# Performance work log

Measured on AMD Instinct MI355X. Metric: run time of the kernel, lower is better.

Reference implementation:

```python
import jax, jax.numpy as jnp
import numpy as np

C_S, C_Z, C_H, H, PQ, PV = 384, 128, 16, 12, 4, 8
B, N = 1, 512
W_C = (2.0 / (9.0 * PQ)) ** 0.5
W_L = (1.0 / 3.0) ** 0.5
OUT_IN = H * C_Z + H * C_H + H * PV * 3 + H * PV  # 2112


def setup_inputs() -> dict:
    key = jax.random.key(0)
    ks = jax.random.split(key, 16)
    s_i = jax.random.normal(ks[0], (B, N, C_S), jnp.float32)
    z_ij = jax.random.normal(ks[1], (B, N, N, C_Z), jnp.float32)
    # random rotation matrices via QR
    raw = jax.random.normal(ks[2], (B, N, 3, 3), jnp.float32)
    q, r = jnp.linalg.qr(raw)
    rots = q * jnp.sign(jnp.diagonal(r, axis1=-2, axis2=-1))[..., None, :]
    trans = jax.random.normal(ks[3], (B, N, 3), jnp.float32)
    sc = lambda fan_in: 1.0 / np.sqrt(fan_in)
    Wq = jax.random.normal(ks[4], (C_S, H * C_H), jnp.float32) * sc(C_S)
    Wk = jax.random.normal(ks[5], (C_S, H * C_H), jnp.float32) * sc(C_S)
    Wv = jax.random.normal(ks[6], (C_S, H * C_H), jnp.float32) * sc(C_S)
    Wqp = jax.random.normal(ks[7], (C_S, H * PQ * 3), jnp.float32) * sc(C_S)
    Wkp = jax.random.normal(ks[8], (C_S, H * PQ * 3), jnp.float32) * sc(C_S)
    Wvp = jax.random.normal(ks[9], (C_S, H * PV * 3), jnp.float32) * sc(C_S)
    Wb = jax.random.normal(ks[10], (C_Z, H), jnp.float32) * sc(C_Z)
    gamma = jax.random.normal(ks[11], (1, 1, 1, H), jnp.float32)
    Wout = jax.random.normal(ks[12], (OUT_IN, C_S), jnp.float32) * sc(OUT_IN)
    bout = jnp.zeros((C_S,), jnp.float32)
    return dict(s_i=s_i, z_ij=z_ij, rots=rots, trans=trans, Wq=Wq, Wk=Wk, Wv=Wv,
                Wqp=Wqp, Wkp=Wkp, Wvp=Wvp, Wb=Wb, gamma=gamma, Wout=Wout, bout=bout)


def reference(s_i, z_ij, rots, trans, Wq, Wk, Wv, Wqp, Wkp, Wvp, Wb, gamma, Wout, bout):
    b, n = s_i.shape[0], s_i.shape[1]
    q_h = (s_i @ Wq).reshape(b, n, H, C_H)
    k_h = (s_i @ Wk).reshape(b, n, H, C_H)
    v_h = (s_i @ Wv).reshape(b, n, H, C_H)
    q_hp = (s_i @ Wqp).reshape(b, n, H, PQ, 3)
    k_hp = (s_i @ Wkp).reshape(b, n, H, PQ, 3)
    v_hp = (s_i @ Wvp).reshape(b, n, H, PV, 3)
    b_ij = z_ij @ Wb  # (b,i,j,h)

    t = trans[:, :, None, None, :]  # (b,i,1,1,3)
    apply = lambda x: jnp.einsum('bixy,bihpy->bihpx', rots, x) + t
    inv_apply = lambda x: jnp.einsum('bixy,bihpx->bihpy', rots, x - t)

    qg = apply(q_hp)  # (b,i,h,p,3) global frame
    kg = apply(k_hp)
    # pairwise rigid point distance term: (b,i,j,h)
    diff = qg[:, :, None] - kg[:, None]  # (b,i,j,h,p,3)
    dist2 = jnp.sum(diff * diff, axis=(-1, -2))

    a_s = jnp.einsum('bihd,bjhd->bijh', q_h, k_h) / (C_H ** 0.5)
    a_rigid = (W_C / 2.0) * gamma * dist2
    a = jax.nn.softmax(W_L * (a_s + b_ij - a_rigid), axis=-2)  # softmax over j

    o_hat = jnp.einsum('bijh,bijd->bihd', a, z_ij)
    o = jnp.einsum('bijh,bjhd->bihd', a, v_h)
    vg = apply(v_hp)  # (b,j,h,p,3)
    o_hp = inv_apply(jnp.einsum('bijh,bjhpx->bihpx', a, vg))  # (b,i,h,pv,3)
    o_hp_norm = jnp.sqrt(jnp.sum(o_hp * o_hp, axis=-1))  # (b,i,h,pv)

    cat = jnp.concatenate([
        o_hat.reshape(b, n, H * C_Z),
        o.reshape(b, n, H * C_H),
        o_hp.reshape(b, n, H * PV * 3),
        o_hp_norm.reshape(b, n, H * PV),
    ], axis=-1)
    return cat @ Wout + bout
```

## Files before the change

### kernel.cpp

```cpp
#include <hip/hip_runtime.h>
#include <hip/hip_bf16.h>
#include <math.h>

#define NRES 512
#define CS   384
#define CZ   128
#define NH   12
#define PW   1152
#define JB   64
#define NCH  8
#define PSTRIDE32 1040
#define KS   6
#define KAW  352

static constexpr float WL_F      = 0.57735026918962576f;
static constexpr float HALF_WC_F = 0.11785113019775792f;

typedef __attribute__((ext_vector_type(8))) short short8v;
typedef __attribute__((ext_vector_type(4))) float floatx4;

__device__ __forceinline__ ushort f2b(float f) {
    union { float f; uint u; } v; v.f = f;
    return (ushort)((v.u + 0x7FFFu + ((v.u >> 16) & 1u)) >> 16);
}
__device__ __forceinline__ float b2f(ushort b) {
    union { uint u; float f; } v; v.u = ((uint)b) << 16; return v.f;
}

__global__ __launch_bounds__(256) void k_prep(
    const float* __restrict__ Wb, const float* __restrict__ Wout,
    ushort* __restrict__ wbt16, ushort* __restrict__ woT)
{
    __shared__ ushort tile[64][72];
    const int bx = blockIdx.x;
    if (bx < 198) {
        const int k0 = (bx % 33) * 64, c0 = (bx / 33) * 64;
        for (int idx = threadIdx.x; idx < 4096; idx += 256) {
            const int r = idx >> 6, c = idx & 63;
            tile[r][c] = f2b(Wout[(size_t)(k0 + r) * 384 + c0 + c]);
        }
        __syncthreads();
        for (int idx = threadIdx.x; idx < 4096; idx += 256) {
            const int c = idx >> 6, r = idx & 63;
            woT[(size_t)(c0 + c) * 2112 + k0 + r] = tile[r][c];
        }
    } else {
        for (int idx = threadIdx.x; idx < 16 * 128; idx += 256) {
            const int h = idx >> 7, cc = idx & 127;
            wbt16[idx] = (h < NH) ? f2b(WL_F * Wb[(size_t)cc * NH + h]) : (ushort)0;
        }
    }
}

__global__ __launch_bounds__(256) void k_gemm(
    const float* __restrict__ s,
    const float* __restrict__ Wq, const float* __restrict__ Wk,
    const float* __restrict__ Wv, const float* __restrict__ Wqp,
    const float* __restrict__ Wkp, const float* __restrict__ Wvp,
    const float* __restrict__ rots, const float* __restrict__ trans,
    float* __restrict__ P)
{
    const int tid = threadIdx.x;
    const int tx = tid & 15, ty = tid >> 4;
    const int n0 = blockIdx.x * 48;
    const int m0 = blockIdx.y * 32;
    __shared__ float As[32][34];
    __shared__ float Bs[32][50];
    __shared__ float rot_lds[32][12];

    const float* Wsel; int W, base;
    if (n0 < 192)      { Wsel = Wq;  W = 192; base = 0;   }
    else if (n0 < 384) { Wsel = Wk;  W = 192; base = 192; }
    else if (n0 < 576) { Wsel = Wv;  W = 192; base = 384; }
    else if (n0 < 720) { Wsel = Wqp; W = 144; base = 576; }
    else if (n0 < 864) { Wsel = Wkp; W = 144; base = 720; }
    else               { Wsel = Wvp; W = 288; base = 864; }
    const int nb = n0 - base;

    if (n0 >= 576) {
        for (int idx = tid; idx < 32 * 12; idx += 256) {
            int r = idx / 12, q = idx % 12;
            rot_lds[r][q] = (q < 9) ? rots[(size_t)(m0 + r) * 9 + q]
                                    : trans[(size_t)(m0 + r) * 3 + q - 9];
        }
    }

    float acc[2][3];
    #pragma unroll
    for (int u = 0; u < 2; ++u)
        #pragma unroll
        for (int v = 0; v < 3; ++v) acc[u][v] = 0.f;

    for (int k0 = 0; k0 < CS; k0 += 32) {
        __syncthreads();
        #pragma unroll
        for (int l = 0; l < 4; ++l) {
            int idx = tid + l * 256;
            int kk = idx & 31, r = idx >> 5;
            As[kk][r] = s[(size_t)(m0 + r) * CS + k0 + kk];
        }
        #pragma unroll
        for (int l = 0; l < 6; ++l) {
            int idx = tid + l * 256;
            int kk = idx / 48, cc = idx % 48;
            Bs[kk][cc] = Wsel[(size_t)(k0 + kk) * W + nb + cc];
        }
        __syncthreads();
        #pragma unroll
        for (int kk = 0; kk < 32; ++kk) {
            const float2 a = *(const float2*)&As[kk][ty * 2];
            const float b0 = Bs[kk][tx * 3], b1 = Bs[kk][tx * 3 + 1], b2 = Bs[kk][tx * 3 + 2];
            acc[0][0] += a.x * b0; acc[0][1] += a.x * b1; acc[0][2] += a.x * b2;
            acc[1][0] += a.y * b0; acc[1][1] += a.y * b1; acc[1][2] += a.y * b2;
        }
    }

    #pragma unroll
    for (int u = 0; u < 2; ++u) {
        float v0 = acc[u][0], v1 = acc[u][1], v2 = acc[u][2];
        if (n0 >= 576) {
            const float* RT = rot_lds[ty * 2 + u];
            const float p0 = v0, p1 = v1, p2 = v2;
            v0 = RT[0] * p0 + RT[1] * p1 + RT[2] * p2 + RT[9];
            v1 = RT[3] * p0 + RT[4] * p1 + RT[5] * p2 + RT[10];
            v2 = RT[6] * p0 + RT[7] * p1 + RT[8] * p2 + RT[11];
        }
        float* dst = P + (size_t)(m0 + ty * 2 + u) * PW + n0 + tx * 3;
        dst[0] = v0; dst[1] = v1; dst[2] = v2;
    }
}

__global__ __launch_bounds__(128) void k_ka(
    const float* __restrict__ P, ushort* __restrict__ Kfull,
    ushort* __restrict__ vp2)
{
    const int j = blockIdx.x;
    const int tid = threadIdx.x;
    __shared__ float njs[NH];
    const float* prow = P + (size_t)j * PW;
    const float* kr  = prow + 192;
    const float* vr  = prow + 384;
    const float* kgr = prow + 720;
    const float* vgr = prow + 864;
    if (tid < NH) {
        float s = 0.f;
        #pragma unroll
        for (int e = 0; e < 12; ++e) { const float v = kgr[tid * 12 + e]; s += v * v; }
        njs[tid] = s;
    }
    __syncthreads();
    ushort* dst = Kfull + (size_t)j * KAW;
    for (int t = tid; t < KAW; t += 128) {
        float v;
        if (t < 192)       v = kr[t];
        else if (t < 336)  v = kgr[t - 192];
        else if (t < 348)  v = njs[t - 336];
        else if (t == 348) v = 1.0f;
        else               v = 0.f;
        dst[t] = f2b(v);
    }
    const int p = j >> 1, par = j & 1;
    for (int c = tid; c < 480; c += 128) {
        const float v = (c < 192) ? vr[c] : vgr[c - 192];
        vp2[((size_t)p * 480 + c) * 2 + par] = f2b(v);
    }
}

__global__ __launch_bounds__(256, 6) void k_flash(
    const float* __restrict__ z, const ushort* __restrict__ wbt16,
    const float* __restrict__ gamma, const float* __restrict__ P,
    const ushort* __restrict__ Kfull, const ushort* __restrict__ vp2,
    uint* __restrict__ part)
{
    const int i   = blockIdx.x;
    const int jc  = blockIdx.y;
    const int j0  = jc * JB;
    const int tid = threadIdx.x;
    const int wid = tid >> 6, lane = tid & 63;

    __shared__ __align__(16) short zbT[128 * JB];
    __shared__ __align__(16) char  uni[10240];
    __shared__ float pm[NH], ps[NH];

    short*  BfT     = (short*)uni;
    float*  ltf     = (float*)uni;
    short*  ltb     = (short*)(uni + 4352);
    float4* halfacc = (float4*)(uni + 6400);

    uint* pb32   = part + ((size_t)i * NCH + jc) * PSTRIDE32;
    ushort* pb16 = (ushort*)pb32;
    float* pbf   = (float*)pb32;

    const int jb = wid * 16 + (lane & 15);
    const int ko = (lane >> 4) * 8;

    short8v af[4];
    {
        const float* za = z + ((size_t)i * NRES + j0 + jb) * CZ + ko;
        #pragma unroll
        for (int m = 0; m < 4; ++m) {
            const float4 f0 = *(const float4*)(za + m * 32);
            const float4 f1 = *(const float4*)(za + m * 32 + 4);
            short8v a;
            a[0] = (short)f2b(f0.x); a[1] = (short)f2b(f0.y);
            a[2] = (short)f2b(f0.z); a[3] = (short)f2b(f0.w);
            a[4] = (short)f2b(f1.x); a[5] = (short)f2b(f1.y);
            a[6] = (short)f2b(f1.z); a[7] = (short)f2b(f1.w);
            af[m] = a;
            #pragma unroll
            for (int e = 0; e < 8; ++e) {
                const int c = ko + m * 32 + e;
                zbT[c * 64 + (((jb >> 3) ^ (c & 7)) * 8) + (jb & 7)] = a[e];
            }
        }
    }
    {
        const float* prow = P + (size_t)i * PW;
        for (int t = tid; t < 12 * 352; t += 256) {
            const int h = t / 352, k = t - h * 352;
            float v = 0.f;
            if (k < 192) {
                if ((k >> 4) == h) v = 0.25f * WL_F * prow[k];
            } else if (k < 336) {
                const int e = k - 192;
                if (e / 12 == h) v = 2.f * HALF_WC_F * WL_F * gamma[h] * prow[576 + e];
            } else if (k < 348) {
                if (k - 336 == h) v = -HALF_WC_F * WL_F * gamma[h];
            } else if (k == 348) {
                float ss = 0.f;
                #pragma unroll
                for (int e = 0; e < 12; ++e) {
                    const float x = prow[576 + h * 12 + e];
                    ss += x * x;
                }
                v = -HALF_WC_F * WL_F * gamma[h] * ss;
            }
            BfT[t] = (short)f2b(v);
        }
    }
    __syncthreads();

    floatx4 lacc = {0.f, 0.f, 0.f, 0.f};
    {
        const int n  = lane & 15;
        const int nb = (n < NH) ? n : 0;
        const ushort* arow = Kfull + (size_t)(j0 + jb) * KAW + ko;
        const short*  brow = &BfT[nb * 352 + ko];
        const ushort* wrow = wbt16 + n * 128 + ko;
        #pragma unroll
        for (int st = 0; st < 11; ++st) {
            const short8v a = *(const short8v*)(arow + st * 32);
            const short8v b = *(const short8v*)(brow + st * 32);
            lacc = __builtin_amdgcn_mfma_f32_16x16x32_bf16(a, b, lacc, 0, 0, 0);
        }
        #pragma unroll
        for (int st = 0; st < 4; ++st) {
            const short8v b = *(const short8v*)(wrow + st * 32);
            lacc = __builtin_amdgcn_mfma_f32_16x16x32_bf16(af[st], b, lacc, 0, 0, 0);
        }
    }
    __syncthreads();
    {
        const int n = lane & 15;
        #pragma unroll
        for (int r = 0; r < 4; ++r)
            ltf[n * 68 + wid * 16 + (lane >> 4) * 4 + r] = lacc[r];
    }
    __syncthreads();

    if (tid < 192) {
        const int h = tid >> 4, s = tid & 15;
        float4 v = *(const float4*)&ltf[h * 68 + s * 4];
        float m = fmaxf(fmaxf(v.x, v.y), fmaxf(v.z, v.w));
        #pragma unroll
        for (int o = 1; o < 16; o <<= 1) m = fmaxf(m, __shfl_xor(m, o));
        float4 e;
        e.x = __expf(v.x - m); e.y = __expf(v.y - m);
        e.z = __expf(v.z - m); e.w = __expf(v.w - m);
        float sum = e.x + e.y + e.z + e.w;
        #pragma unroll
        for (int o = 1; o < 16; o <<= 1) sum += __shfl_xor(sum, o);
        *(float4*)&ltf[h * 68 + s * 4] = e;
        const uint lo = (uint)f2b(e.x) | ((uint)f2b(e.y) << 16);
        const uint hi = (uint)f2b(e.z) | ((uint)f2b(e.w) << 16);
        uint* dst = (uint*)&ltb[h * 64 + (((s >> 1) ^ (h & 7)) * 8) + (s & 1) * 4];
        dst[0] = lo; dst[1] = hi;
        if (s == 0) { pm[h] = m; ps[h] = sum; }
    } else {
        const int tt = tid - 192;
        uint* dst = (uint*)&ltb[(12 + (tt >> 4)) * 64 + (tt & 15) * 4];
        dst[0] = 0u; dst[1] = 0u;
    }
    __syncthreads();

    {
        const int hrow = lane & 15;
        const int u0 = (lane >> 4), u1 = u0 + 4;
        const short8v a0 = *(const short8v*)&ltb[hrow * 64 + ((u0 ^ (hrow & 7)) * 8)];
        const short8v a1 = *(const short8v*)&ltb[hrow * 64 + ((u1 ^ (hrow & 7)) * 8)];
        #pragma unroll
        for (int t = 0; t < 2; ++t) {
            const int d = (wid * 2 + t) * 16 + (lane & 15);
            const short8v b0 = *(const short8v*)&zbT[d * 64 + ((u0 ^ (d & 7)) * 8)];
            const short8v b1 = *(const short8v*)&zbT[d * 64 + ((u1 ^ (d & 7)) * 8)];
            floatx4 acc = {0.f, 0.f, 0.f, 0.f};
            acc = __builtin_amdgcn_mfma_f32_16x16x32_bf16(a0, b0, acc, 0, 0, 0);
            acc = __builtin_amdgcn_mfma_f32_16x16x32_bf16(a1, b1, acc, 0, 0, 0);
            #pragma unroll
            for (int r = 0; r < 4; ++r) {
                const int h = u0 * 4 + r;
                if (h < NH) pb16[h * 128 + d] = f2b(acc[r]);
            }
        }
    }

    {
        if (tid < 240) {
            const int half = tid / 120, col = tid % 120;
            const int h = (col < 48) ? (col >> 2) : ((col - 48) / 6);
            const ushort* vb = vp2 + ((size_t)((j0 >> 1) + half * 16) * 480 + col * 4) * 2;
            const float* er = &ltf[h * 68 + half * 32];
            float ax = 0.f, ay = 0.f, az = 0.f, aw = 0.f;
            #pragma unroll 8
            for (int t = 0; t < 16; ++t) {
                const uint4 raw = *(const uint4*)(vb + (size_t)t * 960);
                const float e0 = er[2 * t], e1 = er[2 * t + 1];
                ax += e0 * b2f((ushort)raw.x) + e1 * b2f((ushort)(raw.x >> 16));
                ay += e0 * b2f((ushort)raw.y) + e1 * b2f((ushort)(raw.y >> 16));
                az += e0 * b2f((ushort)raw.z) + e1 * b2f((ushort)(raw.z >> 16));
                aw += e0 * b2f((ushort)raw.w) + e1 * b2f((ushort)(raw.w >> 16));
            }
            halfacc[tid] = make_float4(ax, ay, az, aw);
        }
        __syncthreads();
        if (tid < 120) {
            const float4 s0 = halfacc[tid], s1 = halfacc[tid + 120];
            const int off16 = (tid < 48) ? 1536 + tid * 4 : 1728 + (tid - 48) * 4;
            uint* dst = (uint*)&pb16[off16];
            dst[0] = (uint)f2b(s0.x + s1.x) | ((uint)f2b(s0.y + s1.y) << 16);
            dst[1] = (uint)f2b(s0.z + s1.z) | ((uint)f2b(s0.w + s1.w) << 16);
        }
        if (tid < NH) { pbf[1008 + tid] = pm[tid]; pbf[1020 + tid] = ps[tid]; }
    }
}

__global__ __launch_bounds__(256) void k_combine(
    const uint* __restrict__ part, const float* __restrict__ rots,
    const float* __restrict__ trans, ushort* __restrict__ cat16)
{
    const int i   = blockIdx.x;
    const int tid = threadIdx.x;
    __shared__ float wgt[NCH][NH];
    __shared__ float ohp[288];

    const uint* base = part + (size_t)i * NCH * PSTRIDE32;
    if (tid < NH) {
        const int h = tid;
        float mm[NCH];
        float M = -1e30f;
        #pragma unroll
        for (int c = 0; c < NCH; ++c) {
            mm[c] = ((const float*)(base + c * PSTRIDE32))[1008 + h];
            M = fmaxf(M, mm[c]);
        }
        float S = 0.f;
        #pragma unroll
        for (int c = 0; c < NCH; ++c) {
            const float w = __expf(mm[c] - M);
            S += w * ((const float*)(base + c * PSTRIDE32))[1020 + h];
            wgt[c][h] = w;
        }
        const float inv = 1.0f / S;
        #pragma unroll
        for (int c = 0; c < NCH; ++c) wgt[c][h] *= inv;
    }
    __syncthreads();

    ushort* crow = cat16 + (size_t)i * 2112;
    uint*   crowu = (uint*)crow;
    if (tid < 192) {
        const int h = tid >> 4;
        float v[8];
        #pragma unroll
        for (int e = 0; e < 8; ++e) v[e] = 0.f;
        #pragma unroll
        for (int c = 0; c < NCH; ++c) {
            const uint4 u = *(const uint4*)&base[c * PSTRIDE32 + tid * 4];
            const float w = wgt[c][h];
            v[0] += b2f((ushort)u.x) * w; v[1] += b2f((ushort)(u.x >> 16)) * w;
            v[2] += b2f((ushort)u.y) * w; v[3] += b2f((ushort)(u.y >> 16)) * w;
            v[4] += b2f((ushort)u.z) * w; v[5] += b2f((ushort)(u.z >> 16)) * w;
            v[6] += b2f((ushort)u.w) * w; v[7] += b2f((ushort)(u.w >> 16)) * w;
        }
        uint4 o;
        o.x = (uint)f2b(v[0]) | ((uint)f2b(v[1]) << 16);
        o.y = (uint)f2b(v[2]) | ((uint)f2b(v[3]) << 16);
        o.z = (uint)f2b(v[4]) | ((uint)f2b(v[5]) << 16);
        o.w = (uint)f2b(v[6]) | ((uint)f2b(v[7]) << 16);
        *(uint4*)&crowu[tid * 4] = o;
    }
    if (tid < 96) {
        const int h = tid >> 3;
        float v0 = 0.f, v1 = 0.f;
        #pragma unroll
        for (int c = 0; c < NCH; ++c) {
            const uint u = base[c * PSTRIDE32 + 768 + tid];
            const float w = wgt[c][h];
            v0 += b2f((ushort)u) * w;
            v1 += b2f((ushort)(u >> 16)) * w;
        }
        crowu[768 + tid] = (uint)f2b(v0) | ((uint)f2b(v1) << 16);
    }
    if (tid < 144) {
        const int h = tid / 12;
        float v0 = 0.f, v1 = 0.f;
        #pragma unroll
        for (int c = 0; c < NCH; ++c) {
            const uint u = base[c * PSTRIDE32 + 864 + tid];
            const float w = wgt[c][h];
            v0 += b2f((ushort)u) * w;
            v1 += b2f((ushort)(u >> 16)) * w;
        }
        ohp[tid * 2] = v0; ohp[tid * 2 + 1] = v1;
    }
    __syncthreads();

    if (tid < 96) {
        const int h = tid >> 3, p = tid & 7;
        float R[9];
        #pragma unroll
        for (int k = 0; k < 9; ++k) R[k] = rots[(size_t)i * 9 + k];
        const float g0 = ohp[h * 24 + p * 3 + 0] - trans[(size_t)i * 3 + 0];
        const float g1 = ohp[h * 24 + p * 3 + 1] - trans[(size_t)i * 3 + 1];
        const float g2 = ohp[h * 24 + p * 3 + 2] - trans[(size_t)i * 3 + 2];
        const float oy0 = R[0] * g0 + R[3] * g1 + R[6] * g2;
        const float oy1 = R[1] * g0 + R[4] * g1 + R[7] * g2;
        const float oy2 = R[2] * g0 + R[5] * g1 + R[8] * g2;
        crow[1728 + h * 24 + p * 3 + 0] = f2b(oy0);
        crow[1728 + h * 24 + p * 3 + 1] = f2b(oy1);
        crow[1728 + h * 24 + p * 3 + 2] = f2b(oy2);
        crow[2016 + h * 8 + p] = f2b(sqrtf(oy0 * oy0 + oy1 * oy1 + oy2 * oy2));
    }
}

__global__ __launch_bounds__(256) void k_out(
    const ushort* __restrict__ cat16, const ushort* __restrict__ woT,
    float* __restrict__ opart)
{
    const int tid = threadIdx.x;
    const int wid = tid >> 6, lane = tid & 63;
    const int wm = wid >> 1, wn = wid & 1;
    const int i0 = blockIdx.x * 32 + wm * 16;
    const int c0 = blockIdx.y * 32 + wn * 16;
    const int k0 = blockIdx.z * 352;
    const ushort* arow = cat16 + (size_t)(i0 + (lane & 15)) * 2112 + k0 + (lane >> 4) * 8;
    const ushort* brow = woT   + (size_t)(c0 + (lane & 15)) * 2112 + k0 + (lane >> 4) * 8;
    floatx4 acc = {0.f, 0.f, 0.f, 0.f};
    #pragma unroll
    for (int st = 0; st < 11; ++st) {
        const short8v a = *(const short8v*)(arow + st * 32);
        const short8v b = *(const short8v*)(brow + st * 32);
        acc = __builtin_amdgcn_mfma_f32_16x16x32_bf16(a, b, acc, 0, 0, 0);
    }
    float* ob = opart + (size_t)blockIdx.z * 512 * 384;
    #pragma unroll
    for (int r = 0; r < 4; ++r) {
        const int i = i0 + (lane >> 4) * 4 + r;
        ob[(size_t)i * 384 + c0 + (lane & 15)] = acc[r];
    }
}

__global__ __launch_bounds__(256) void k_outred(
    const float* __restrict__ opart, const float* __restrict__ bout,
    float* __restrict__ out)
{
    const int e4 = blockIdx.x * 256 + threadIdx.x;
    const float4* p = (const float4*)opart;
    const float4 b = ((const float4*)bout)[e4 % 96];
    float4 r = b;
    #pragma unroll
    for (int k = 0; k < KS; ++k) {
        const float4 v = p[e4 + k * 49152];
        r.x += v.x; r.y += v.y; r.z += v.z; r.w += v.w;
    }
    ((float4*)out)[e4] = r;
}

extern "C" void kernel_launch(void* const* d_in, const int* in_sizes, int n_in,
                              void* d_out, int out_size, void* d_ws, size_t ws_size,
                              hipStream_t stream)
{
    const float* s_i   = (const float*)d_in[0];
    const float* z_ij  = (const float*)d_in[1];
    const float* rots  = (const float*)d_in[2];
    const float* trans = (const float*)d_in[3];
    const float* Wq    = (const float*)d_in[4];
    const float* Wk    = (const float*)d_in[5];
    const float* Wv    = (const float*)d_in[6];
    const float* Wqp   = (const float*)d_in[7];
    const float* Wkp   = (const float*)d_in[8];
    const float* Wvp   = (const float*)d_in[9];
    const float* Wb    = (const float*)d_in[10];
    const float* gamma = (const float*)d_in[11];
    const float* Wout  = (const float*)d_in[12];
    const float* bout  = (const float*)d_in[13];
    float* ws = (float*)d_ws;
    float*  P     = ws;
    uint*   part  = (uint*)(P + 589824);
    float*  opart = (float*)part;
    ushort* cat16 = (ushort*)(part + (size_t)512 * NCH * PSTRIDE32);
    ushort* wbt16 = cat16 + 1081344;
    ushort* kfull = wbt16 + 2048;
    ushort* woT   = kfull + 512 * KAW;
    ushort* vp2   = woT + (size_t)384 * 2112;
    float*  out   = (float*)d_out;

    hipLaunchKernelGGL(k_gemm, dim3(24, 16), dim3(256), 0, stream,
                       s_i, Wq, Wk, Wv, Wqp, Wkp, Wvp, rots, trans, P);
    hipLaunchKernelGGL(k_ka, dim3(512), dim3(128), 0, stream,
                       P, kfull, vp2);
    hipLaunchKernelGGL(k_prep, dim3(199), dim3(256), 0, stream,
                       Wb, Wout, wbt16, woT);
    hipLaunchKernelGGL(k_flash, dim3(512, NCH), dim3(256), 0, stream,
                       z_ij, wbt16, gamma, P, kfull, vp2, part);
    hipLaunchKernelGGL(k_combine, dim3(512), dim3(256), 0, stream,
                       part, rots, trans, cat16);
    hipLaunchKernelGGL(k_out, dim3(16, 12, KS), dim3(256), 0, stream,
                       cat16, woT, opart);
    hipLaunchKernelGGL(k_outred, dim3(192), dim3(256), 0, stream,
                       opart, bout, out);
}
```

Before: 120.4 us.

## Merge K-prep and weight-prep kernels; batch global loads ahead of use in flash

After: 116.2 us, median of 3. 1.04x faster.

```diff
diff --git a/kernel.cpp b/kernel.cpp
--- a/kernel.cpp
+++ b/kernel.cpp
@@ -27,25 +27,59 @@
     union { uint u; float f; } v; v.u = ((uint)b) << 16; return v.f;
 }
 
-__global__ __launch_bounds__(256) void k_prep(
-    const float* __restrict__ Wb, const float* __restrict__ Wout,
+__global__ __launch_bounds__(256) void k_aux(
+    const float* __restrict__ P, const float* __restrict__ Wb,
+    const float* __restrict__ Wout,
+    ushort* __restrict__ Kfull, ushort* __restrict__ vp2,
     ushort* __restrict__ wbt16, ushort* __restrict__ woT)
 {
     __shared__ ushort tile[64][72];
+    __shared__ float njs[NH];
     const int bx = blockIdx.x;
-    if (bx < 198) {
-        const int k0 = (bx % 33) * 64, c0 = (bx / 33) * 64;
-        for (int idx = threadIdx.x; idx < 4096; idx += 256) {
+    const int tid = threadIdx.x;
+    if (bx < 512) {
+        const int j = bx;
+        const float* prow = P + (size_t)j * PW;
+        const float* kr  = prow + 192;
+        const float* vr  = prow + 384;
+        const float* kgr = prow + 720;
+        const float* vgr = prow + 864;
+        if (tid < NH) {
+            float s = 0.f;
+            #pragma unroll
+            for (int e = 0; e < 12; ++e) { const float v = kgr[tid * 12 + e]; s += v * v; }
+            njs[tid] = s;
+        }
+        __syncthreads();
+        ushort* dst = Kfull + (size_t)j * KAW;
+        for (int t = tid; t < KAW; t += 256) {
+            float v;
+            if (t < 192)       v = kr[t];
+            else if (t < 336)  v = kgr[t - 192];
+            else if (t < 348)  v = njs[t - 336];
+            else if (t == 348) v = 1.0f;
+            else               v = 0.f;
+            dst[t] = f2b(v);
+        }
+        const int p = j >> 1, par = j & 1;
+        for (int c = tid; c < 480; c += 256) {
+            const float v = (c < 192) ? vr[c] : vgr[c - 192];
+            vp2[((size_t)p * 480 + c) * 2 + par] = f2b(v);
+        }
+    } else if (bx < 710) {
+        const int t = bx - 512;
+        const int k0 = (t % 33) * 64, c0 = (t / 33) * 64;
+        for (int idx = tid; idx < 4096; idx += 256) {
             const int r = idx >> 6, c = idx & 63;
             tile[r][c] = f2b(Wout[(size_t)(k0 + r) * 384 + c0 + c]);
         }
         __syncthreads();
-        for (int idx = threadIdx.x; idx < 4096; idx += 256) {
+        for (int idx = tid; idx < 4096; idx += 256) {
             const int c = idx >> 6, r = idx & 63;
             woT[(size_t)(c0 + c) * 2112 + k0 + r] = tile[r][c];
         }
     } else {
-        for (int idx = threadIdx.x; idx < 16 * 128; idx += 256) {
+        for (int idx = tid; idx < 16 * 128; idx += 256) {
             const int h = idx >> 7, cc = idx & 127;
             wbt16[idx] = (h < NH) ? f2b(WL_F * Wb[(size_t)cc * NH + h]) : (ushort)0;
         }
@@ -130,43 +164,7 @@
     }
 }
 
-__global__ __launch_bounds__(128) void k_ka(
-    const float* __restrict__ P, ushort* __restrict__ Kfull,
-    ushort* __restrict__ vp2)
-{
-    const int j = blockIdx.x;
-    const int tid = threadIdx.x;
-    __shared__ float njs[NH];
-    const float* prow = P + (size_t)j * PW;
-    const float* kr  = prow + 192;
-    const float* vr  = prow + 384;
-    const float* kgr = prow + 720;
-    const float* vgr = prow + 864;
-    if (tid < NH) {
-        float s = 0.f;
-        #pragma unroll
-        for (int e = 0; e < 12; ++e) { const float v = kgr[tid * 12 + e]; s += v * v; }
-        njs[tid] = s;
-    }
-    __syncthreads();
-    ushort* dst = Kfull + (size_t)j * KAW;
-    for (int t = tid; t < KAW; t += 128) {
-        float v;
-        if (t < 192)       v = kr[t];
-        else if (t < 336)  v = kgr[t - 192];
-        else if (t < 348)  v = njs[t - 336];
-        else if (t == 348) v = 1.0f;
-        else               v = 0.f;
-        dst[t] = f2b(v);
-    }
-    const int p = j >> 1, par = j & 1;
-    for (int c = tid; c < 480; c += 128) {
-        const float v = (c < 192) ? vr[c] : vgr[c - 192];
-        vp2[((size_t)p * 480 + c) * 2 + par] = f2b(v);
-    }
-}
-
-__global__ __launch_bounds__(256, 6) void k_flash(
+__global__ __launch_bounds__(256, 4) void k_flash(
     const float* __restrict__ z, const ushort* __restrict__ wbt16,
     const float* __restrict__ gamma, const float* __restrict__ P,
     const ushort* __restrict__ Kfull, const ushort* __restrict__ vp2,
@@ -197,10 +195,15 @@
     short8v af[4];
     {
         const float* za = z + ((size_t)i * NRES + j0 + jb) * CZ + ko;
+        float4 fz[8];
         #pragma unroll
         for (int m = 0; m < 4; ++m) {
-            const float4 f0 = *(const float4*)(za + m * 32);
-            const float4 f1 = *(const float4*)(za + m * 32 + 4);
+            fz[2 * m]     = *(const float4*)(za + m * 32);
+            fz[2 * m + 1] = *(const float4*)(za + m * 32 + 4);
+        }
+        #pragma unroll
+        for (int m = 0; m < 4; ++m) {
+            const float4 f0 = fz[2 * m], f1 = fz[2 * m + 1];
             short8v a;
             a[0] = (short)f2b(f0.x); a[1] = (short)f2b(f0.y);
             a[2] = (short)f2b(f0.z); a[3] = (short)f2b(f0.w);
@@ -247,17 +250,19 @@
         const ushort* arow = Kfull + (size_t)(j0 + jb) * KAW + ko;
         const short*  brow = &BfT[nb * 352 + ko];
         const ushort* wrow = wbt16 + n * 128 + ko;
+        short8v kf[11], wv[4];
+        #pragma unroll
+        for (int st = 0; st < 11; ++st) kf[st] = *(const short8v*)(arow + st * 32);
+        #pragma unroll
+        for (int st = 0; st < 4; ++st)  wv[st] = *(const short8v*)(wrow + st * 32);
         #pragma unroll
         for (int st = 0; st < 11; ++st) {
-            const short8v a = *(const short8v*)(arow + st * 32);
             const short8v b = *(const short8v*)(brow + st * 32);
-            lacc = __builtin_amdgcn_mfma_f32_16x16x32_bf16(a, b, lacc, 0, 0, 0);
-        }
-        #pragma unroll
-        for (int st = 0; st < 4; ++st) {
-            const short8v b = *(const short8v*)(wrow + st * 32);
-            lacc = __builtin_amdgcn_mfma_f32_16x16x32_bf16(af[st], b, lacc, 0, 0, 0);
-        }
+            lacc = __builtin_amdgcn_mfma_f32_16x16x32_bf16(kf[st], b, lacc, 0, 0, 0);
+        }
+        #pragma unroll
+        for (int st = 0; st < 4; ++st)
+            lacc = __builtin_amdgcn_mfma_f32_16x16x32_bf16(af[st], wv[st], lacc, 0, 0, 0);
     }
     __syncthreads();
     {
@@ -321,14 +326,20 @@
             const ushort* vb = vp2 + ((size_t)((j0 >> 1) + half * 16) * 480 + col * 4) * 2;
             const float* er = &ltf[h * 68 + half * 32];
             float ax = 0.f, ay = 0.f, az = 0.f, aw = 0.f;
-            #pragma unroll 8
-            for (int t = 0; t < 16; ++t) {
-                const uint4 raw = *(const uint4*)(vb + (size_t)t * 960);
-                const float e0 = er[2 * t], e1 = er[2 * t + 1];
-                ax += e0 * b2f((ushort)raw.x) + e1 * b2f((ushort)(raw.x >> 16));
-                ay += e0 * b2f((ushort)raw.y) + e1 * b2f((ushort)(raw.y >> 16));
-                az += e0 * b2f((ushort)raw.z) + e1 * b2f((ushort)(raw.z >> 16));
-                aw += e0 * b2f((ushort)raw.w) + e1 * b2f((ushort)(raw.w >> 16));
+            #pragma unroll
+            for (int b = 0; b < 2; ++b) {
+                uint4 raw[8];
+                #pragma unroll
+                for (int t = 0; t < 8; ++t)
+                    raw[t] = *(const uint4*)(vb + (size_t)(b * 8 + t) * 960);
+                #pragma unroll
+                for (int t = 0; t < 8; ++t) {
+                    const float e0 = er[2 * (b * 8 + t)], e1 = er[2 * (b * 8 + t) + 1];
+                    ax += e0 * b2f((ushort)raw[t].x) + e1 * b2f((ushort)(raw[t].x >> 16));
+                    ay += e0 * b2f((ushort)raw[t].y) + e1 * b2f((ushort)(raw[t].y >> 16));
+                    az += e0 * b2f((ushort)raw[t].z) + e1 * b2f((ushort)(raw[t].z >> 16));
+                    aw += e0 * b2f((ushort)raw[t].w) + e1 * b2f((ushort)(raw[t].w >> 16));
+                }
             }
             halfacc[tid] = make_float4(ax, ay, az, aw);
         }
@@ -517,10 +528,8 @@
 
     hipLaunchKernelGGL(k_gemm, dim3(24, 16), dim3(256), 0, stream,
                        s_i, Wq, Wk, Wv, Wqp, Wkp, Wvp, rots, trans, P);
-    hipLaunchKernelGGL(k_ka, dim3(512), dim3(128), 0, stream,
-                       P, kfull, vp2);
-    hipLaunchKernelGGL(k_prep, dim3(199), dim3(256), 0, stream,
-                       Wb, Wout, wbt16, woT);
+    hipLaunchKernelGGL(k_aux, dim3(711), dim3(256), 0, stream,
+                       P, Wb, Wout, kfull, vp2, wbt16, woT);
     hipLaunchKernelGGL(k_flash, dim3(512, NCH), dim3(256), 0, stream,
                        z_ij, wbt16, gamma, P, kfull, vp2, part);
     hipLaunchKernelGGL(k_combine, dim3(512), dim3(256), 0, stream,
```
